# Performance work log

Measured on AMD Instinct MI355X. Metric: run time of the kernel, lower is better.

## Reference

```python
import jax, jax.numpy as jnp
import numpy as np

N = 50000      # nodes
E = 500000     # edges per etype
IN_DIM = 128
HID = 64
NUM_CLASSES = 2
NUM_ETYPES = 3


def setup_inputs() -> dict:
    key = jax.random.key(0)
    ks = jax.random.split(key, 16)
    feat = jax.random.normal(ks[0], (N, IN_DIM), dtype=jnp.float32)
    edges = {}
    for i in range(NUM_ETYPES):
        edges[f"src{i}"] = jax.random.randint(ks[1 + 2 * i], (E,), 0, N, dtype=jnp.int32)
        edges[f"dst{i}"] = jax.random.randint(ks[2 + 2 * i], (E,), 0, N, dtype=jnp.int32)
    # learned params
    Wm = jax.random.normal(ks[8], (IN_DIM, NUM_CLASSES), dtype=jnp.float32) / np.sqrt(IN_DIM)
    bm = jnp.zeros((NUM_CLASSES,), jnp.float32)
    W0 = jax.random.normal(ks[9], (IN_DIM, HID), dtype=jnp.float32) / np.sqrt(IN_DIM)
    b0 = jnp.zeros((HID,), jnp.float32)
    W1 = jax.random.normal(ks[10], (HID, NUM_CLASSES), dtype=jnp.float32) / np.sqrt(HID)
    b1 = jnp.zeros((NUM_CLASSES,), jnp.float32)
    p0 = jnp.full((NUM_ETYPES,), 0.5, jnp.float32)  # layer-0 per-etype weights
    p1 = jnp.full((NUM_ETYPES,), 0.5, jnp.float32)  # layer-1 per-etype weights
    return dict(feat=feat, Wm=Wm, bm=bm, W0=W0, b0=b0, W1=W1, b1=b1,
                p0=p0, p1=p1, **edges)


def _segment_mean(x, dst, n):
    # mean of incoming messages per destination node
    s = jax.ops.segment_sum(x, dst, num_segments=n)
    cnt = jax.ops.segment_sum(jnp.ones((dst.shape[0], 1), x.dtype), dst, num_segments=n)
    return s / jnp.maximum(cnt, 1.0)


def _care_layer(feat, srcs, dsts, p, W, b):
    n = feat.shape[0]
    # per-etype copy_u -> mean aggregation, then activation (tanh)
    h = jnp.zeros((n, feat.shape[1]), feat.dtype)
    for i, (s, d) in enumerate(zip(srcs, dsts)):
        hr = jnp.tanh(_segment_mean(feat[s], d, n))
        h = h + p[i] * hr
    h = jnp.tanh(h + feat)  # residual + activation
    return h @ W + b


def reference(feat, Wm, bm, W0, b0, W1, b1, p0, p1,
              src0, dst0, src1, dst1, src2, dst2):
    sim = jnp.tanh(feat @ Wm + bm)  # layer-0 MLP on dst features
    srcs = (src0, src1, src2)
    dsts = (dst0, dst1, dst2)
    h = _care_layer(feat, srcs, dsts, p0, W0, b0)   # [N, HID]
    out = _care_layer(h, srcs, dsts, p1, W1, b1)    # [N, C]
    return (out, sim)
```

## Files before the change

### kernel.cpp

```cpp
#include <hip/hip_runtime.h>

#define NN 50000
#define EE 500000
#define FD 128
#define HD 64
#define NET 3
#define CSTRIDE 650000

#define CVT_BLKS   (NN / 4)
#define CNT_BLKS   ((NET * EE + 255) / 256)
#define PREP_BLKS  (CVT_BLKS + CNT_BLKS + 1)

__device__ __forceinline__ unsigned short f2bf(float f) {
    union { float f; unsigned int i; } c; c.f = f;
    unsigned int u = c.i;
    return (unsigned short)((u + 0x7fffu + ((u >> 16) & 1u)) >> 16);
}
__device__ __forceinline__ float tanh_fast(float x) {
    float e = __expf(2.0f * x);
    return 1.0f - __fdividef(2.0f, e + 1.0f);
}
__device__ __forceinline__ float bflo(unsigned int u) { return __uint_as_float(u << 16); }
__device__ __forceinline__ float bfhiA(unsigned int u) { return __uint_as_float(u); }
__device__ __forceinline__ float bfhiX(unsigned int u) { return __uint_as_float(u & 0xffff0000u); }

__global__ void k_prepcount(const float* __restrict__ feat, unsigned short* __restrict__ featb,
                            unsigned short* __restrict__ h1b,
                            const float* __restrict__ Wm, const float* __restrict__ bm,
                            float* __restrict__ simout,
                            const int* __restrict__ d0, const int* __restrict__ d1,
                            const int* __restrict__ d2, int* __restrict__ cnt) {
    int bid = blockIdx.x;
    if (bid < CVT_BLKS) {
        int w    = threadIdx.x >> 6;
        int lane = threadIdx.x & 63;
        int row  = bid * 4 + w;
        const float2 f = *(const float2*)(feat + (size_t)row * FD + lane * 2);
        ushort2 o; o.x = f2bf(f.x); o.y = f2bf(f.y);
        *(ushort2*)(featb + (size_t)row * FD + lane * 2) = o;
        float sp0 = f.x * Wm[(lane * 2) * 2 + 0] + f.y * Wm[(lane * 2 + 1) * 2 + 0];
        float sp1 = f.x * Wm[(lane * 2) * 2 + 1] + f.y * Wm[(lane * 2 + 1) * 2 + 1];
        #pragma unroll
        for (int off = 1; off <= 32; off <<= 1) {
            sp0 += __shfl_xor(sp0, off, 64);
            sp1 += __shfl_xor(sp1, off, 64);
        }
        if (lane == 0) {
            simout[row * 2 + 0] = tanh_fast(sp0 + bm[0]);
            simout[row * 2 + 1] = tanh_fast(sp1 + bm[1]);
        }
    } else if (bid < CVT_BLKS + CNT_BLKS) {
        int e = (bid - CVT_BLKS) * 256 + threadIdx.x;
        if (e < NET * EE) {
            int et = e / EE;
            int i  = e - et * EE;
            const int* d = (et == 0) ? d0 : ((et == 1) ? d1 : d2);
            atomicAdd(&cnt[et * NN + d[i]], 1);
        }
    } else {
        int t = threadIdx.x;
        if (t < 32) *(ushort4*)(featb + (size_t)NN * FD + t * 4) = make_ushort4(0, 0, 0, 0);
        else if (t < 48) {
            int i = t - 32;
            *(ushort4*)(h1b + (size_t)NN * HD + i * 4) = make_ushort4(0, 0, 0, 0);
        }
    }
}

__global__ void k_scan1(const int* __restrict__ cnt, int* __restrict__ bsum) {
    int et = blockIdx.x / 50, b = blockIdx.x % 50;
    const int* c = cnt + et * NN + b * 1000;
    __shared__ int sh[256];
    int t = threadIdx.x;
    int s = 0;
    for (int i = t; i < 1000; i += 256) s += (c[i] + 3) & ~3;
    sh[t] = s; __syncthreads();
    for (int off = 128; off > 0; off >>= 1) {
        if (t < off) sh[t] += sh[t + off];
        __syncthreads();
    }
    if (t == 0) bsum[blockIdx.x] = sh[0];
}
__global__ void k_scan3(const int* __restrict__ cnt, const int* __restrict__ bsum,
                        int* __restrict__ rowptr, int* __restrict__ cursor,
                        int* __restrict__ col, float* __restrict__ invd) {
    int blk = blockIdx.x;
    int et = blk / 50, b = blk % 50;
    int boff = 0;
    for (int q = 0; q < b; ++q) boff += bsum[et * 50 + q];
    const int* c = cnt + et * NN + b * 1000;
    __shared__ int sh[256];
    int t = threadIdx.x;
    int i0 = t * 4;
    int c4[4] = {0, 0, 0, 0};
    int s = 0;
    if (i0 < 1000) {
        #pragma unroll
        for (int q = 0; q < 4; ++q) { int v = c[i0 + q]; c4[q] = v; s += (v + 3) & ~3; }
    }
    sh[t] = s; __syncthreads();
    for (int off = 1; off < 256; off <<= 1) {
        int add = (t >= off) ? sh[t - off] : 0;
        __syncthreads();
        sh[t] += add;
        __syncthreads();
    }
    int run = boff + sh[t] - s;
    if (i0 < 1000) {
        int* rp = rowptr + et * (NN + 1);
        int* cu = cursor + et * NN;
        int* cl = col + et * CSTRIDE;
        float* iv = invd + et * NN;
        int node0 = b * 1000 + i0;
        #pragma unroll
        for (int q = 0; q < 4; ++q) {
            int node = node0 + q; int v = c4[q]; int pv = (v + 3) & ~3;
            rp[node] = run; cu[node] = run;
            iv[node] = 1.0f / (float)((v > 0) ? v : 1);
            for (int k = v; k < pv; ++k) cl[run + k] = NN;
            run += pv;
        }
        if (b == 49 && t == 249) rp[NN] = run;
    }
}

__global__ void k_scatter(const int* __restrict__ s0, const int* __restrict__ d0,
                          const int* __restrict__ s1, const int* __restrict__ d1,
                          const int* __restrict__ s2, const int* __restrict__ d2,
                          int* __restrict__ cursor, int* __restrict__ col) {
    int t = blockIdx.x * 256 + threadIdx.x;
    if (t >= NET * EE) return;
    int et = t / EE;
    int e  = t - et * EE;
    const int* s = (et == 0) ? s0 : ((et == 1) ? s1 : s2);
    const int* d = (et == 0) ? d0 : ((et == 1) ? d1 : d2);
    int dd = d[e];
    int pos = atomicAdd(&cursor[et * NN + dd], 1);
    col[(size_t)et * CSTRIDE + pos] = s[e];
}


__global__ __launch_bounds__(256) void k_layer0(
    const float* __restrict__ feat, const unsigned short* __restrict__ featb,
    const float* __restrict__ W0, const float* __restrict__ b0, const float* __restrict__ p0,
    const int* __restrict__ rowptr, const int* __restrict__ col,
    const float* __restrict__ invd,
    unsigned short* __restrict__ h1b) {
    __shared__ float hbuf[4][FD];
    int w    = threadIdx.x >> 6;
    int lane = threadIdx.x & 63;
    int s    = lane >> 4;
    int i    = lane & 15;
    int d8   = i * 8;
    int node = (int)blockIdx.x * 4 + w;

    const float2 fr = *(const float2*)(feat + (size_t)node * FD + d8 + 2 * s);

    float a0 = 0.f, a1 = 0.f;
    #pragma unroll
    for (int et = 0; et < NET; ++et) {
        const int* rp = rowptr + et * (NN + 1);
        int st = rp[node], t = rp[node + 1];
        const int* cc = col + (size_t)et * CSTRIDE;
        float x0 = 0.f, x1 = 0.f, x2 = 0.f, x3 = 0.f;
        float x4 = 0.f, x5 = 0.f, x6 = 0.f, x7 = 0.f;
        for (int base = st; base < t; base += 64) {
            int my = cc[base + lane];
            int m = t - base; if (m > 64) m = 64;
            int j = 0;
            for (; j + 8 <= m; j += 8) {
                int eA = __shfl(my, j + s, 64);
                int eB = __shfl(my, j + 4 + s, 64);
                uint4 uA = *(const uint4*)(featb + (size_t)eA * FD + d8);
                uint4 uB = *(const uint4*)(featb + (size_t)eB * FD + d8);
                x0 += bflo(uA.x); x1 += bfhiA(uA.x); x2 += bflo(uA.y); x3 += bfhiA(uA.y);
                x4 += bflo(uA.z); x5 += bfhiA(uA.z); x6 += bflo(uA.w); x7 += bfhiA(uA.w);
                x0 += bflo(uB.x); x1 += bfhiA(uB.x); x2 += bflo(uB.y); x3 += bfhiA(uB.y);
                x4 += bflo(uB.z); x5 += bfhiA(uB.z); x6 += bflo(uB.w); x7 += bfhiA(uB.w);
            }
            if (j < m) {
                int eA = __shfl(my, j + s, 64);
                uint4 uA = *(const uint4*)(featb + (size_t)eA * FD + d8);
                x0 += bflo(uA.x); x1 += bfhiA(uA.x); x2 += bflo(uA.y); x3 += bfhiA(uA.y);
                x4 += bflo(uA.z); x5 += bfhiA(uA.z); x6 += bflo(uA.w); x7 += bfhiA(uA.w);
            }
        }
        x0 += __shfl_xor(x0, 16, 64); x0 += __shfl_xor(x0, 32, 64);
        x1 += __shfl_xor(x1, 16, 64); x1 += __shfl_xor(x1, 32, 64);
        x2 += __shfl_xor(x2, 16, 64); x2 += __shfl_xor(x2, 32, 64);
        x3 += __shfl_xor(x3, 16, 64); x3 += __shfl_xor(x3, 32, 64);
        x4 += __shfl_xor(x4, 16, 64); x4 += __shfl_xor(x4, 32, 64);
        x5 += __shfl_xor(x5, 16, 64); x5 += __shfl_xor(x5, 32, 64);
        x6 += __shfl_xor(x6, 16, 64); x6 += __shfl_xor(x6, 32, 64);
        x7 += __shfl_xor(x7, 16, 64); x7 += __shfl_xor(x7, 32, 64);
        float v0 = (s & 2) ? ((s & 1) ? x6 : x4) : ((s & 1) ? x2 : x0);
        float v1 = (s & 2) ? ((s & 1) ? x7 : x5) : ((s & 1) ? x3 : x1);
        float inv = invd[et * NN + node];
        float pe = p0[et];
        a0 += pe * tanh_fast(v0 * inv);
        a1 += pe * tanh_fast(v1 * inv);
    }
    float h0v = tanh_fast(a0 + fr.x);
    float h1v = tanh_fast(a1 + fr.y);

    *(float2*)&hbuf[w][d8 + 2 * s] = make_float2(h0v, h1v);
    float o = b0[lane];
    #pragma unroll 8
    for (int k4 = 0; k4 < FD; k4 += 4) {
        float4 hv = *(const float4*)&hbuf[w][k4];
        o = fmaf(hv.x, W0[(k4 + 0) * HD + lane], o);
        o = fmaf(hv.y, W0[(k4 + 1) * HD + lane], o);
        o = fmaf(hv.z, W0[(k4 + 2) * HD + lane], o);
        o = fmaf(hv.w, W0[(k4 + 3) * HD + lane], o);
    }
    h1b[(size_t)node * HD + lane] = f2bf(o);
}

__global__ __launch_bounds__(256) void k_layer1(
    const unsigned short* __restrict__ h1b,
    const float* __restrict__ W1, const float* __restrict__ b1,
    const float* __restrict__ p1, const int* __restrict__ rowptr,
    const int* __restrict__ col, const float* __restrict__ invd,
    float* __restrict__ out) {
    int w    = threadIdx.x >> 6;
    int lane = threadIdx.x & 63;
    int s    = lane >> 4;
    int i    = lane & 15;
    int d4   = i * 4;
    int node = (int)blockIdx.x * 4 + w;

    uint2 hr = *(const uint2*)(h1b + (size_t)node * HD + d4);

    float a = 0.f;
    #pragma unroll
    for (int et = 0; et < NET; ++et) {
        const int* rp = rowptr + et * (NN + 1);
        int st = rp[node], t = rp[node + 1];
        const int* cc = col + (size_t)et * CSTRIDE;
        float x0 = 0.f, x1 = 0.f, x2 = 0.f, x3 = 0.f;
        for (int base = st; base < t; base += 64) {
            int my = cc[base + lane];
            int m = t - base; if (m > 64) m = 64;
            int j = 0;
            for (; j + 8 <= m; j += 8) {
                int eA = __shfl(my, j + s, 64);
                int eB = __shfl(my, j + 4 + s, 64);
                uint2 uA = *(const uint2*)(h1b + (size_t)eA * HD + d4);
                uint2 uB = *(const uint2*)(h1b + (size_t)eB * HD + d4);
                x0 += bflo(uA.x); x1 += bfhiA(uA.x); x2 += bflo(uA.y); x3 += bfhiA(uA.y);
                x0 += bflo(uB.x); x1 += bfhiA(uB.x); x2 += bflo(uB.y); x3 += bfhiA(uB.y);
            }
            if (j < m) {
                int eA = __shfl(my, j + s, 64);
                uint2 uA = *(const uint2*)(h1b + (size_t)eA * HD + d4);
                x0 += bflo(uA.x); x1 += bfhiA(uA.x); x2 += bflo(uA.y); x3 += bfhiA(uA.y);
            }
        }
        x0 += __shfl_xor(x0, 16, 64); x0 += __shfl_xor(x0, 32, 64);
        x1 += __shfl_xor(x1, 16, 64); x1 += __shfl_xor(x1, 32, 64);
        x2 += __shfl_xor(x2, 16, 64); x2 += __shfl_xor(x2, 32, 64);
        x3 += __shfl_xor(x3, 16, 64); x3 += __shfl_xor(x3, 32, 64);
        float v = (s & 2) ? ((s & 1) ? x3 : x2) : ((s & 1) ? x1 : x0);
        float inv = invd[et * NN + node];
        a += p1[et] * tanh_fast(v * inv);
    }
    float r0 = bflo(hr.x), r1 = bfhiX(hr.x), r2 = bflo(hr.y), r3 = bfhiX(hr.y);
    float r = (s & 2) ? ((s & 1) ? r3 : r2) : ((s & 1) ? r1 : r0);
    float g = tanh_fast(a + r);

    int dim = d4 + s;
    float q0 = g * W1[dim * 2 + 0];
    float q1 = g * W1[dim * 2 + 1];
    #pragma unroll
    for (int off = 1; off <= 32; off <<= 1) {
        q0 += __shfl_xor(q0, off, 64);
        q1 += __shfl_xor(q1, off, 64);
    }
    if (lane == 0) {
        out[node * 2 + 0] = q0 + b1[0];
        out[node * 2 + 1] = q1 + b1[1];
    }
}


extern "C" void kernel_launch(void* const* d_in, const int* in_sizes, int n_in,
                              void* d_out, int out_size, void* d_ws, size_t ws_size,
                              hipStream_t stream) {
    const float* feat = (const float*)d_in[0];
    const float* Wm   = (const float*)d_in[1];
    const float* bm   = (const float*)d_in[2];
    const float* W0   = (const float*)d_in[3];
    const float* b0   = (const float*)d_in[4];
    const float* W1   = (const float*)d_in[5];
    const float* b1   = (const float*)d_in[6];
    const float* p0   = (const float*)d_in[7];
    const float* p1   = (const float*)d_in[8];
    const int* src0 = (const int*)d_in[9];
    const int* dst0 = (const int*)d_in[10];
    const int* src1 = (const int*)d_in[11];
    const int* dst1 = (const int*)d_in[12];
    const int* src2 = (const int*)d_in[13];
    const int* dst2 = (const int*)d_in[14];

    char* ws = (char*)d_ws;
    int*            cnt    = (int*)(ws + 0);
    int*            rowptr = (int*)(ws + 600000);
    int*            cursor = (int*)(ws + 1200016);
    float*          invd   = (float*)(ws + 1800016);
    int*            bsum   = (int*)(ws + 2400016);
    int*            col    = (int*)(ws + 2400624);
    unsigned short* featb  = (unsigned short*)(ws + 10200880);
    unsigned short* h1b    = (unsigned short*)(ws + 23001136);

    float* out = (float*)d_out;
    float* sim = out + (size_t)NN * 2;

    hipMemsetAsync(cnt, 0, sizeof(int) * NET * NN, stream);
    k_prepcount<<<PREP_BLKS, 256, 0, stream>>>(feat, featb, h1b, Wm, bm, sim,
                                               dst0, dst1, dst2, cnt);
    k_scan1<<<150, 256, 0, stream>>>(cnt, bsum);
    k_scan3<<<150, 256, 0, stream>>>(cnt, bsum, rowptr, cursor, col, invd);
    k_scatter<<<(NET * EE + 255) / 256, 256, 0, stream>>>(src0, dst0, src1, dst1, src2, dst2,
                                                          cursor, col);
    k_layer0<<<NN / 4, 256, 0, stream>>>(feat, featb, W0, b0, p0,
                                         rowptr, col, invd, h1b);
    k_layer1<<<NN / 4, 256, 0, stream>>>(h1b, W1, b1, p1, rowptr, col, invd, out);
}
```

Measured before the change: 326.8 us.

## Two-pass bucketed CSR scatter to localize atomic and col writes

Replaces the single random scatter of edges into CSR with a two-pass scheme. Edges are first bucketed by destination block of 128 nodes into a packed (src<<16|dst) buffer using per-bucket atomics. A second pass then scatters from that buffer, so consecutive threads hit nearby cursor and col addresses. This adds an extra kernel, a small scan, a second counting atomic, and an intermediate buffer of 1.5M words. The intent is better cache locality for the atomics and stores.

```diff
diff --git a/kernel.cpp b/kernel.cpp
--- a/kernel.cpp
+++ b/kernel.cpp
@@ -6,6 +6,7 @@
 #define HD 64
 #define NET 3
 #define CSTRIDE 650000
+#define NBK 391
 
 #define CVT_BLKS   (NN / 4)
 #define CNT_BLKS   ((NET * EE + 255) / 256)
@@ -29,7 +30,8 @@
                             const float* __restrict__ Wm, const float* __restrict__ bm,
                             float* __restrict__ simout,
                             const int* __restrict__ d0, const int* __restrict__ d1,
-                            const int* __restrict__ d2, int* __restrict__ cnt) {
+                            const int* __restrict__ d2, int* __restrict__ cnt,
+                            int* __restrict__ bcnt) {
     int bid = blockIdx.x;
     if (bid < CVT_BLKS) {
         int w    = threadIdx.x >> 6;
@@ -55,7 +57,9 @@
             int et = e / EE;
             int i  = e - et * EE;
             const int* d = (et == 0) ? d0 : ((et == 1) ? d1 : d2);
-            atomicAdd(&cnt[et * NN + d[i]], 1);
+            int dd = d[i];
+            atomicAdd(&cnt[et * NN + dd], 1);
+            atomicAdd(&bcnt[et * NBK + (dd >> 7)], 1);
         }
     } else {
         int t = threadIdx.x;
@@ -65,6 +69,49 @@
             *(ushort4*)(h1b + (size_t)NN * HD + i * 4) = make_ushort4(0, 0, 0, 0);
         }
     }
+}
+
+__global__ void k_bscan(const int* __restrict__ bcnt, int* __restrict__ bcur) {
+    __shared__ int sh[512];
+    int et = blockIdx.x;
+    int t = threadIdx.x;
+    int v = (t < NBK) ? bcnt[et * NBK + t] : 0;
+    sh[t] = v; __syncthreads();
+    for (int off = 1; off < 512; off <<= 1) {
+        int add = (t >= off) ? sh[t - off] : 0;
+        __syncthreads();
+        sh[t] += add;
+        __syncthreads();
+    }
+    if (t < NBK) bcur[et * NBK + t] = et * EE + sh[t] - v;
+}
+
+__global__ void k_bucket(const int* __restrict__ s0, const int* __restrict__ d0,
+                         const int* __restrict__ s1, const int* __restrict__ d1,
+                         const int* __restrict__ s2, const int* __restrict__ d2,
+                         int* __restrict__ bcur, unsigned int* __restrict__ ebuf) {
+    int t = blockIdx.x * 256 + threadIdx.x;
+    if (t >= NET * EE) return;
+    int et = t / EE;
+    int e  = t - et * EE;
+    const int* s = (et == 0) ? s0 : ((et == 1) ? s1 : s2);
+    const int* d = (et == 0) ? d0 : ((et == 1) ? d1 : d2);
+    unsigned int ss = (unsigned int)s[e];
+    unsigned int dd = (unsigned int)d[e];
+    int pos = atomicAdd(&bcur[et * NBK + (dd >> 7)], 1);
+    ebuf[pos] = (ss << 16) | dd;
+}
+
+__global__ void k_scatter2(const unsigned int* __restrict__ ebuf,
+                           int* __restrict__ cursor, int* __restrict__ col) {
+    int t = blockIdx.x * 256 + threadIdx.x;
+    if (t >= NET * EE) return;
+    int et = (t >= EE) + (t >= 2 * EE);
+    unsigned int u = ebuf[t];
+    int dd = (int)(u & 0xffffu);
+    int ss = (int)(u >> 16);
+    int pos = atomicAdd(&cursor[et * NN + dd], 1);
+    col[(size_t)et * CSTRIDE + pos] = ss;
 }
 
 __global__ void k_scan1(const int* __restrict__ cnt, int* __restrict__ bsum) {
@@ -122,21 +169,6 @@
         }
         if (b == 49 && t == 249) rp[NN] = run;
     }
-}
-
-__global__ void k_scatter(const int* __restrict__ s0, const int* __restrict__ d0,
-                          const int* __restrict__ s1, const int* __restrict__ d1,
-                          const int* __restrict__ s2, const int* __restrict__ d2,
-                          int* __restrict__ cursor, int* __restrict__ col) {
-    int t = blockIdx.x * 256 + threadIdx.x;
-    if (t >= NET * EE) return;
-    int et = t / EE;
-    int e  = t - et * EE;
-    const int* s = (et == 0) ? s0 : ((et == 1) ? s1 : s2);
-    const int* d = (et == 0) ? d0 : ((et == 1) ? d1 : d2);
-    int dd = d[e];
-    int pos = atomicAdd(&cursor[et * NN + dd], 1);
-    col[(size_t)et * CSTRIDE + pos] = s[e];
 }
 
 
@@ -304,24 +336,29 @@
 
     char* ws = (char*)d_ws;
     int*            cnt    = (int*)(ws + 0);
-    int*            rowptr = (int*)(ws + 600000);
-    int*            cursor = (int*)(ws + 1200016);
-    float*          invd   = (float*)(ws + 1800016);
-    int*            bsum   = (int*)(ws + 2400016);
-    int*            col    = (int*)(ws + 2400624);
-    unsigned short* featb  = (unsigned short*)(ws + 10200880);
-    unsigned short* h1b    = (unsigned short*)(ws + 23001136);
+    int*            bcnt   = (int*)(ws + 600000);
+    int*            rowptr = (int*)(ws + 604704);
+    int*            cursor = (int*)(ws + 1204720);
+    float*          invd   = (float*)(ws + 1804720);
+    int*            bsum   = (int*)(ws + 2404720);
+    int*            bcur   = (int*)(ws + 2405328);
+    int*            col    = (int*)(ws + 2410032);
+    unsigned int*   ebuf   = (unsigned int*)(ws + 10210288);
+    unsigned short* featb  = (unsigned short*)(ws + 16210288);
+    unsigned short* h1b    = (unsigned short*)(ws + 29010544);
 
     float* out = (float*)d_out;
     float* sim = out + (size_t)NN * 2;
 
-    hipMemsetAsync(cnt, 0, sizeof(int) * NET * NN, stream);
+    hipMemsetAsync(cnt, 0, 604704, stream);
     k_prepcount<<<PREP_BLKS, 256, 0, stream>>>(feat, featb, h1b, Wm, bm, sim,
-                                               dst0, dst1, dst2, cnt);
+                                               dst0, dst1, dst2, cnt, bcnt);
+    k_bscan<<<NET, 512, 0, stream>>>(bcnt, bcur);
     k_scan1<<<150, 256, 0, stream>>>(cnt, bsum);
     k_scan3<<<150, 256, 0, stream>>>(cnt, bsum, rowptr, cursor, col, invd);
-    k_scatter<<<(NET * EE + 255) / 256, 256, 0, stream>>>(src0, dst0, src1, dst1, src2, dst2,
-                                                          cursor, col);
+    k_bucket<<<(NET * EE + 255) / 256, 256, 0, stream>>>(src0, dst0, src1, dst1, src2, dst2,
+                                                         bcur, ebuf);
+    k_scatter2<<<(NET * EE + 255) / 256, 256, 0, stream>>>(ebuf, cursor, col);
     k_layer0<<<NN / 4, 256, 0, stream>>>(feat, featb, W0, b0, p0,
                                          rowptr, col, invd, h1b);
     k_layer1<<<NN / 4, 256, 0, stream>>>(h1b, W1, b1, p1, rowptr, col, invd, out);
```

Result: slower. 995.5 us (+204.6%).
